# Kernel optimization log

Hardware: AMD Instinct MI355X
Metric: run time of the kernel (lower is better)

The kernel has to match this reference:

```python
import jax, jax.numpy as jnp
import numpy as np

B, C, F, T = 4, 64, 257, 256
H, OUT = 256, 64

def setup_inputs() -> dict:
    key = jax.random.key(0)
    ks = jax.random.split(key, 7)
    w = lambda k, shape: jax.random.normal(k, shape, dtype=jnp.float32) * 0.05
    return {
        "x": jax.random.normal(ks[0], (B, C, F, T), dtype=jnp.float32),
        "W_ih": w(ks[1], (4 * H, C)),   # torch LSTM weight_ih_l0, gate order i,f,g,o
        "W_hh": w(ks[2], (4 * H, H)),   # weight_hh_l0
        "b_ih": w(ks[3], (4 * H,)),
        "b_hh": w(ks[4], (4 * H,)),
        "W_lin": w(ks[5], (OUT, H)),
        "b_lin": w(ks[6], (OUT,)),
    }

def _lstm(y, W_ih, W_hh, b_ih, b_hh):
    # y: (N, T, C) -> (N, T, H); PyTorch gate order i, f, g, o
    N, Tl, _ = y.shape
    Hd = W_hh.shape[1]
    # precompute input contributions for all timesteps in one big GEMM
    x_gates = jnp.einsum('ntc,gc->ntg', y, W_ih) + b_ih + b_hh  # (N, T, 4H)

    def step(carry, xg):
        h, c = carry
        g = xg + h @ W_hh.T  # (N, 4H)
        i, f, gg, o = jnp.split(g, 4, axis=-1)
        c = jax.nn.sigmoid(f) * c + jax.nn.sigmoid(i) * jnp.tanh(gg)
        h = jax.nn.sigmoid(o) * jnp.tanh(c)
        return (h, c), h

    h0 = jnp.zeros((N, Hd), y.dtype)
    _, hs = jax.lax.scan(step, (h0, h0), jnp.swapaxes(x_gates, 0, 1))  # (T, N, H)
    return jnp.swapaxes(hs, 0, 1)  # (N, T, H)

def reference(x, W_ih, W_hh, b_ih, b_hh, W_lin, b_lin):
    b, c, f, t = x.shape
    y = x.transpose(0, 2, 3, 1).reshape(b * f, t, c)  # (B*F, T, C)
    h = _lstm(y, W_ih, W_hh, b_ih, b_hh)              # (B*F, T, H)
    out = h @ W_lin.T + b_lin                          # (B*F, T, OUT)
    return out.reshape(b, f, t, -1).transpose(0, 3, 1, 2)  # (B, OUT, F, T)
```

## Files before the change

kernel.cpp:

```cpp
#include <hip/hip_runtime.h>

#define NSEQ 1028
#define TT   256
#define CC   64
#define HH   256
#define SLABE 32768
#define XROW 528
#define XG_A (16*XROW)
#define XG_LDS (2*XG_A + 2*SLABE*2)
#define AROWB 656
#define FB_LDS (2*16*AROWB + 2*SLABE*2)
#define OUTP_LDS (128*264*2 + 64*264*2)

typedef unsigned short u16;
typedef float  f32x4 __attribute__((ext_vector_type(4)));
typedef __bf16 v8bf  __attribute__((ext_vector_type(8)));

__device__ __forceinline__ u16 f2bf(float f){
  unsigned u = __builtin_bit_cast(unsigned, f);
  u += 0x7FFFu + ((u >> 16) & 1u);
  return (u16)(u >> 16);
}
__device__ __forceinline__ float sigm(float x){
  float t = __builtin_amdgcn_exp2f(-1.4426950408889634f * x);
  return __builtin_amdgcn_rcpf(1.0f + t);
}
__device__ __forceinline__ float tanh_f(float x){
  float a = __builtin_fabsf(x);
  float t = __builtin_amdgcn_exp2f(-2.885390081777927f * a);
  float r = (1.0f - t) * __builtin_amdgcn_rcpf(1.0f + t);
  return __builtin_copysignf(r, x);
}
__device__ __forceinline__ void mfma_a(f32x4& d, v8bf a, v8bf b){
  asm("v_mfma_f32_16x16x32_bf16 %0, %1, %2, %0" : "+v"(d) : "v"(a), "a"(b));
}
__device__ __forceinline__ void mfma_v(f32x4& d, v8bf a, v8bf b){
  asm("v_mfma_f32_16x16x32_bf16 %0, %1, %2, %0" : "+v"(d) : "v"(a), "v"(b));
}
__device__ __forceinline__ void soft_barrier(){
  asm volatile("s_waitcnt lgkmcnt(0)" ::: "memory");
  __builtin_amdgcn_sched_barrier(0);
  __builtin_amdgcn_s_barrier();
  __builtin_amdgcn_sched_barrier(0);
}

__global__ void k_pack_w(const float* __restrict__ Whh, const float* __restrict__ Wih,
                         u16* __restrict__ wpack){
  int idx = blockIdx.x*256 + threadIdx.x;
  if (idx >= 10*SLABE) return;
  int j    = idx & 7;
  int lane = (idx >> 3) & 63;
  int ct   = (idx >> 9) & 7;
  int w    = (idx >> 12) & 7;
  int kt   = idx >> 15;
  int col  = (ct >> 1)*256 + w*32 + (ct & 1)*16 + (lane & 15);
  int k    = kt*32 + (lane >> 4)*8 + j;
  float v  = (k < 256) ? Whh[col*256 + k] : Wih[col*64 + (k - 256)];
  wpack[idx] = f2bf(v);
}

__global__ void k_bias(const float* __restrict__ bi, const float* __restrict__ bh,
                       float* __restrict__ bias){
  int i = blockIdx.x*256 + threadIdx.x;
  if (i < 1024) bias[i] = bi[i] + bh[i];
}

__global__ void k_wlin(const float* __restrict__ Wl, u16* __restrict__ wlin){
  int i = blockIdx.x*256 + threadIdx.x;
  if (i >= 64*264) return;
  int col = i / 264, k = i % 264;
  wlin[i] = (k < 256) ? f2bf(Wl[col*256 + k]) : (u16)0;
}

__global__ void k_ytrans(const float* __restrict__ x, u16* __restrict__ ybuf){
  __shared__ u16 tile[64][257];
  int n = blockIdx.x, b = n / 257, f = n % 257, tid = threadIdx.x;
  for (int i = tid; i < 64*256; i += 256){
    int c = i >> 8, t = i & 255;
    tile[c][t] = f2bf(x[((size_t)(b*64 + c)*257 + f)*256 + t]);
  }
  __syncthreads();
  for (int i = tid; i < 256*64; i += 256){
    int t = i >> 6, c = i & 63;
    ybuf[((size_t)n*256 + t)*64 + c] = tile[c][t];
  }
}

__global__ __launch_bounds__(512) void k_xgates(const u16* __restrict__ wpack,
      const float* __restrict__ bias, const u16* __restrict__ ybuf,
      u16* __restrict__ xgs, int t0, int CH){
  __shared__ u16 yt[16*16*72];
  const int g = blockIdx.x, tb = blockIdx.y*16, n0 = g*16;
  const int tid = threadIdx.x, lane = tid & 63, w = tid >> 6;
  const int l15 = lane & 15, q = lane >> 4;

  v8bf wf[2][8];
  #pragma unroll
  for (int kf = 0; kf < 2; ++kf)
    #pragma unroll
    for (int ct = 0; ct < 8; ++ct)
      wf[kf][ct] = *(const v8bf*)(wpack + (((8 + kf)*8 + w)*8 + ct)*512 + lane*8);
  float biasr[8];
  #pragma unroll
  for (int ct = 0; ct < 8; ++ct)
    biasr[ct] = bias[(ct >> 1)*256 + w*32 + (ct & 1)*16 + l15];

  #pragma unroll
  for (int s = 0; s < 4; ++s){
    int i = tid + s*512;
    int seq = i >> 7, tt = (i >> 3) & 15, c8 = i & 7;
    uint4 v = {0u,0u,0u,0u};
    if (n0 + seq < NSEQ)
      v = *(const uint4*)(ybuf + ((size_t)(n0 + seq)*TT + t0 + tb + tt)*64 + c8*8);
    *(uint4*)(yt + tt*1152 + seq*72 + c8*8) = v;
  }
  __syncthreads();

  for (int tt = 0; tt < 16; ++tt){
    f32x4 acc[8];
    #pragma unroll
    for (int ct = 0; ct < 8; ++ct)
      acc[ct] = (f32x4){biasr[ct], biasr[ct], biasr[ct], biasr[ct]};
    v8bf a0 = *(const v8bf*)(yt + tt*1152 + l15*72 + q*8);
    v8bf a1 = *(const v8bf*)(yt + tt*1152 + l15*72 + 32 + q*8);
    #pragma unroll
    for (int ct = 0; ct < 8; ++ct){
      acc[ct] = __builtin_amdgcn_mfma_f32_16x16x32_bf16(a0, wf[0][ct], acc[ct], 0, 0, 0);
      acc[ct] = __builtin_amdgcn_mfma_f32_16x16x32_bf16(a1, wf[1][ct], acc[ct], 0, 0, 0);
    }
    unsigned dw[16];
    #pragma unroll
    for (int ct = 0; ct < 8; ++ct)
      #pragma unroll
      for (int p = 0; p < 2; ++p)
        dw[ct*2 + p] = (unsigned)f2bf(acc[ct][2*p]) | ((unsigned)f2bf(acc[ct][2*p + 1]) << 16);
    u16* dst = xgs + ((((size_t)g*CH + tb + tt)*8 + w)*64 + lane)*32;
    *(uint4*)(dst +  0) = (uint4){dw[0], dw[1], dw[2], dw[3]};
    *(uint4*)(dst +  8) = (uint4){dw[4], dw[5], dw[6], dw[7]};
    *(uint4*)(dst + 16) = (uint4){dw[8], dw[9], dw[10], dw[11]};
    *(uint4*)(dst + 24) = (uint4){dw[12], dw[13], dw[14], dw[15]};
  }
}

__global__ __launch_bounds__(512, 2) void k_lstm_xg(const u16* __restrict__ wpack,
      const u16* __restrict__ xgs, u16* __restrict__ hbuf, float* __restrict__ cbuf,
      int t0, int CH){
  extern __shared__ char smem[];
  char* lA = smem;
  u16*  lW = (u16*)(smem + 2*XG_A);
  const int tid = threadIdx.x, lane = tid & 63, w = tid >> 6;
  const int g = blockIdx.x, n0 = g*16;
  const int l15 = lane & 15, q = lane >> 4;
  const int srow = tid >> 5, schunk = tid & 31;

  v8bf wreg[4][8];
  #pragma unroll
  for (int kt = 0; kt < 4; ++kt)
    #pragma unroll
    for (int ct = 0; ct < 8; ++ct)
      wreg[kt][ct] = *(const v8bf*)(wpack + ((kt*8 + w)*8 + ct)*512 + lane*8);
  {
    const uint4* src = (const uint4*)(wpack + 4*SLABE);
    uint4* dst = (uint4*)lW;
    for (int i = tid; i < (2*SLABE)/8; i += 512) dst[i] = src[i];
  }
  {
    uint4 hv = {0u,0u,0u,0u};
    if (t0 > 0 && n0 + srow < NSEQ)
      hv = *(const uint4*)(hbuf + ((size_t)(n0 + srow)*TT + (t0 - 1))*HH + schunk*8);
    *(uint4*)(lA + (t0 & 1)*XG_A + srow*XROW + schunk*16) = hv;
  }
  f32x4 creg[2];
  creg[0] = (f32x4){0.f,0.f,0.f,0.f};
  creg[1] = (f32x4){0.f,0.f,0.f,0.f};
  if (t0 > 0){
    #pragma unroll
    for (int u = 0; u < 2; ++u)
      #pragma unroll
      for (int j = 0; j < 4; ++j){
        int row = 4*q + j, unit = w*32 + u*16 + l15;
        if (n0 + row < NSEQ) creg[u][j] = cbuf[(size_t)(n0 + row)*HH + unit];
      }
  }
  __syncthreads();

  const u16* wp = wpack;

  v8bf sbuf[8];
  uint4 xgv[4];
  {
    const u16* wpw0 = wp + w*4096 + lane*8;
    #pragma unroll
    for (int ct = 0; ct < 8; ++ct) sbuf[ct] = *(const v8bf*)(wpw0 + 6*SLABE + ct*512);
    const u16* xb = xgs + ((((size_t)g*CH + 0)*8 + w)*64 + lane)*32;
    xgv[0] = *(const uint4*)(xb +  0);
    xgv[1] = *(const uint4*)(xb +  8);
    xgv[2] = *(const uint4*)(xb + 16);
    xgv[3] = *(const uint4*)(xb + 24);
  }

  for (int t = t0; t < t0 + CH; ++t){
    char* Acur = lA + (t & 1)*XG_A;
    char* Anxt = lA + ((t + 1) & 1)*XG_A;
    asm("" : "+s"(wp));
    const u16* wpw = wp + w*4096 + lane*8;

    if (t > t0 && n0 + srow < NSEQ){
      uint4 hv = *(const uint4*)(Acur + srow*XROW + schunk*16);
      *(uint4*)(hbuf + ((size_t)(n0 + srow)*TT + (t - 1))*HH + schunk*8) = hv;
    }

    f32x4 acc[8];
    #pragma unroll
    for (int ct = 0; ct < 8; ++ct){
      #pragma unroll
      for (int p = 0; p < 2; ++p){
        unsigned u = ((const unsigned*)&xgv[(ct*2 + p) >> 2])[(ct*2 + p) & 3];
        acc[ct][2*p]     = __builtin_bit_cast(float, u << 16);
        acc[ct][2*p + 1] = __builtin_bit_cast(float, u & 0xffff0000u);
      }
    }
    asm volatile("s_nop 1"
      : "+v"(acc[0]), "+v"(acc[1]), "+v"(acc[2]), "+v"(acc[3]),
        "+v"(acc[4]), "+v"(acc[5]), "+v"(acc[6]), "+v"(acc[7]));

    if (t + 1 < t0 + CH){
      const u16* xb = xgs + ((((size_t)g*CH + (t + 1 - t0))*8 + w)*64 + lane)*32;
      xgv[0] = *(const uint4*)(xb +  0);
      xgv[1] = *(const uint4*)(xb +  8);
      xgv[2] = *(const uint4*)(xb + 16);
      xgv[3] = *(const uint4*)(xb + 24);
    }
    __builtin_amdgcn_sched_barrier(0);

    #define AFRAGX(kt) (*(const v8bf*)(Acur + l15*XROW + (kt)*64 + q*16))
    #define LFRAGX(kt,ct) (*(const v8bf*)(lW + (((kt)-4)*8 + w)*4096 + (ct)*512 + lane*8))

    { v8bf a = AFRAGX(6);
      #pragma unroll
      for (int ct = 0; ct < 8; ++ct) mfma_v(acc[ct], a, sbuf[ct]);
      #pragma unroll
      for (int ct = 0; ct < 8; ++ct) sbuf[ct] = *(const v8bf*)(wpw + 7*SLABE + ct*512);
      __builtin_amdgcn_sched_barrier(0); }
    { v8bf a = AFRAGX(0);
      #pragma unroll
      for (int ct = 0; ct < 8; ++ct) mfma_a(acc[ct], a, wreg[0][ct]); }
    { v8bf a = AFRAGX(1);
      #pragma unroll
      for (int ct = 0; ct < 8; ++ct) mfma_a(acc[ct], a, wreg[1][ct]); }
    { v8bf a = AFRAGX(2);
      #pragma unroll
      for (int ct = 0; ct < 8; ++ct) mfma_a(acc[ct], a, wreg[2][ct]); }
    { v8bf a = AFRAGX(3);
      #pragma unroll
      for (int ct = 0; ct < 8; ++ct) mfma_a(acc[ct], a, wreg[3][ct]); }
    { v8bf a = AFRAGX(4);
      #pragma unroll
      for (int ct = 0; ct < 8; ++ct) mfma_v(acc[ct], a, LFRAGX(4,ct)); }
    { v8bf a = AFRAGX(5);
      #pragma unroll
      for (int ct = 0; ct < 8; ++ct) mfma_v(acc[ct], a, LFRAGX(5,ct)); }
    { v8bf a = AFRAGX(7);
      #pragma unroll
      for (int ct = 0; ct < 8; ++ct) mfma_v(acc[ct], a, sbuf[ct]);
      #pragma unroll
      for (int ct = 0; ct < 8; ++ct) sbuf[ct] = *(const v8bf*)(wpw + 6*SLABE + ct*512);
      __builtin_amdgcn_sched_barrier(0); }

    asm volatile("s_nop 7\n\ts_nop 7\n\ts_nop 7"
      : "+v"(acc[0]), "+v"(acc[1]), "+v"(acc[2]), "+v"(acc[3]),
        "+v"(acc[4]), "+v"(acc[5]), "+v"(acc[6]), "+v"(acc[7]));

    #pragma unroll
    for (int u = 0; u < 2; ++u){
      #pragma unroll
      for (int j = 0; j < 4; ++j){
        float xi = acc[0 + u][j], xf = acc[2 + u][j], xg = acc[4 + u][j], xo = acc[6 + u][j];
        float cv = sigm(xf)*creg[u][j] + sigm(xi)*tanh_f(xg);
        float hv = sigm(xo)*tanh_f(cv);
        creg[u][j] = cv;
        int row = 4*q + j, unit = w*32 + u*16 + l15;
        *(u16*)(Anxt + row*XROW + unit*2) = f2bf(hv);
      }
    }
    soft_barrier();
  }
  {
    char* Afin = lA + ((t0 + CH) & 1)*XG_A;
    if (n0 + srow < NSEQ){
      uint4 hv = *(const uint4*)(Afin + srow*XROW + schunk*16);
      *(uint4*)(hbuf + ((size_t)(n0 + srow)*TT + (t0 + CH - 1))*HH + schunk*8) = hv;
    }
    #pragma unroll
    for (int u = 0; u < 2; ++u)
      #pragma unroll
      for (int j = 0; j < 4; ++j){
        int row = 4*q + j, unit = w*32 + u*16 + l15;
        if (n0 + row < NSEQ) cbuf[(size_t)(n0 + row)*HH + unit] = creg[u][j];
      }
  }
}

__global__ __launch_bounds__(512, 2) void k_lstm_fb(const u16* __restrict__ wpack,
      const float* __restrict__ bias, const u16* __restrict__ ybuf,
      u16* __restrict__ hbuf){
  extern __shared__ char smem[];
  char* lA = smem;
  u16*  lW = (u16*)(smem + 2*16*AROWB);
  const int tid = threadIdx.x, lane = tid & 63, w = tid >> 6;
  const int n0 = blockIdx.x * 16;
  const int l15 = lane & 15, q = lane >> 4;
  const int srow = tid >> 5, schunk = tid & 31;

  v8bf wreg[4][8];
  #pragma unroll
  for (int kt = 0; kt < 4; ++kt)
    #pragma unroll
    for (int ct = 0; ct < 8; ++ct)
      wreg[kt][ct] = *(const v8bf*)(wpack + ((kt*8 + w)*8 + ct)*512 + lane*8);
  {
    const uint4* src = (const uint4*)(wpack + 4*SLABE);
    uint4* dst = (uint4*)lW;
    for (int i = tid; i < (2*SLABE)/8; i += 512) dst[i] = src[i];
  }
  float biasr[8];
  #pragma unroll
  for (int ct = 0; ct < 8; ++ct)
    biasr[ct] = bias[(ct >> 1)*256 + w*32 + (ct & 1)*16 + l15];
  {
    unsigned* z = (unsigned*)lA;
    for (int i = tid; i < (2*16*AROWB)/4; i += 512) z[i] = 0;
  }
  __syncthreads();
  {
    unsigned v = 0;
    if (n0 + srow < NSEQ)
      v = *(const unsigned*)(ybuf + ((size_t)(n0 + srow)*TT + 0)*64 + schunk*2);
    *(unsigned*)(lA + srow*AROWB + 512 + schunk*4) = v;
  }
  f32x4 creg[2];
  creg[0] = (f32x4){0.f,0.f,0.f,0.f};
  creg[1] = (f32x4){0.f,0.f,0.f,0.f};
  __syncthreads();

  const u16* wp = wpack;
  v8bf sbuf[8];
  {
    const u16* wpw0 = wp + w*4096 + lane*8;
    #pragma unroll
    for (int ct = 0; ct < 8; ++ct) sbuf[ct] = *(const v8bf*)(wpw0 + 6*SLABE + ct*512);
  }

  for (int t = 0; t < TT; ++t){
    char* Acur = lA + (t & 1)*16*AROWB;
    char* Anxt = lA + ((t + 1) & 1)*16*AROWB;
    asm("" : "+s"(wp));
    const u16* wpw = wp + w*4096 + lane*8;

    unsigned yv = 0;
    if (t + 1 < TT && n0 + srow < NSEQ)
      yv = *(const unsigned*)(ybuf + ((size_t)(n0 + srow)*TT + (t + 1))*64 + schunk*2);

    if (t >= 1 && n0 + srow < NSEQ){
      uint4 hv = *(const uint4*)(Acur + srow*AROWB + schunk*16);
      *(uint4*)(hbuf + ((size_t)(n0 + srow)*TT + (t - 1))*HH + schunk*8) = hv;
    }

    f32x4 acc[8];
    #pragma unroll
    for (int ct = 0; ct < 8; ++ct)
      acc[ct] = (f32x4){biasr[ct], biasr[ct], biasr[ct], biasr[ct]};
    asm volatile("s_nop 1"
      : "+v"(acc[0]), "+v"(acc[1]), "+v"(acc[2]), "+v"(acc[3]),
        "+v"(acc[4]), "+v"(acc[5]), "+v"(acc[6]), "+v"(acc[7]));

    #define AFRAG(kt) (*(const v8bf*)(Acur + l15*AROWB + (kt)*64 + q*16))
    #define LFRAG(kt,ct) (*(const v8bf*)(lW + (((kt)-4)*8 + w)*4096 + (ct)*512 + lane*8))

    { v8bf a = AFRAG(0);
      #pragma unroll
      for (int ct = 0; ct < 8; ++ct) mfma_a(acc[ct], a, wreg[0][ct]); }
    { v8bf a = AFRAG(1);
      #pragma unroll
      for (int ct = 0; ct < 8; ++ct) mfma_a(acc[ct], a, wreg[1][ct]); }
    { v8bf a = AFRAG(6);
      #pragma unroll
      for (int ct = 0; ct < 8; ++ct) mfma_v(acc[ct], a, sbuf[ct]);
      #pragma unroll
      for (int ct = 0; ct < 8; ++ct) sbuf[ct] = *(const v8bf*)(wpw + 7*SLABE + ct*512);
      __builtin_amdgcn_sched_barrier(0); }
    { v8bf a = AFRAG(2);
      #pragma unroll
      for (int ct = 0; ct < 8; ++ct) mfma_a(acc[ct], a, wreg[2][ct]); }
    { v8bf a = AFRAG(3);
      #pragma unroll
      for (int ct = 0; ct < 8; ++ct) mfma_a(acc[ct], a, wreg[3][ct]); }
    { v8bf a = AFRAG(7);
      #pragma unroll
      for (int ct = 0; ct < 8; ++ct) mfma_v(acc[ct], a, sbuf[ct]);
      #pragma unroll
      for (int ct = 0; ct < 8; ++ct) sbuf[ct] = *(const v8bf*)(wpw + 8*SLABE + ct*512);
      __builtin_amdgcn_sched_barrier(0); }
    { v8bf a = AFRAG(4);
      #pragma unroll
      for (int ct = 0; ct < 8; ++ct) mfma_v(acc[ct], a, LFRAG(4,ct)); }
    { v8bf a = AFRAG(8);
      #pragma unroll
      for (int ct = 0; ct < 8; ++ct) mfma_v(acc[ct], a, sbuf[ct]);
      #pragma unroll
      for (int ct = 0; ct < 8; ++ct) sbuf[ct] = *(const v8bf*)(wpw + 9*SLABE + ct*512);
      __builtin_amdgcn_sched_barrier(0); }
    { v8bf a = AFRAG(5);
      #pragma unroll
      for (int ct = 0; ct < 8; ++ct) mfma_v(acc[ct], a, LFRAG(5,ct)); }
    { v8bf a = AFRAG(9);
      #pragma unroll
      for (int ct = 0; ct < 8; ++ct) mfma_v(acc[ct], a, sbuf[ct]);
      #pragma unroll
      for (int ct = 0; ct < 8; ++ct) sbuf[ct] = *(const v8bf*)(wpw + 6*SLABE + ct*512);
      __builtin_amdgcn_sched_barrier(0); }

    asm volatile("s_nop 7\n\ts_nop 7\n\ts_nop 7"
      : "+v"(acc[0]), "+v"(acc[1]), "+v"(acc[2]), "+v"(acc[3]),
        "+v"(acc[4]), "+v"(acc[5]), "+v"(acc[6]), "+v"(acc[7]));

    #pragma unroll
    for (int u = 0; u < 2; ++u){
      #pragma unroll
      for (int j = 0; j < 4; ++j){
        float xi = acc[0 + u][j], xf = acc[2 + u][j], xg = acc[4 + u][j], xo = acc[6 + u][j];
        float cv = sigm(xf)*creg[u][j] + sigm(xi)*tanh_f(xg);
        float hv = sigm(xo)*tanh_f(cv);
        creg[u][j] = cv;
        int row = 4*q + j, unit = w*32 + u*16 + l15;
        *(u16*)(Anxt + row*AROWB + unit*2) = f2bf(hv);
      }
    }
    if (t + 1 < TT)
      *(unsigned*)(Anxt + srow*AROWB + 512 + schunk*4) = yv;
    soft_barrier();
  }
  {
    char* Afin = lA + (TT & 1)*16*AROWB;
    if (n0 + srow < NSEQ){
      uint4 hv = *(const uint4*)(Afin + srow*AROWB + schunk*16);
      *(uint4*)(hbuf + ((size_t)(n0 + srow)*TT + (TT - 1))*HH + schunk*8) = hv;
    }
  }
}

__global__ __launch_bounds__(256) void k_outproj(const u16* __restrict__ hbuf,
      const u16* __restrict__ wlin, const float* __restrict__ blin,
      float* __restrict__ out){
  extern __shared__ char smem[];
  u16* sA = (u16*)smem;
  u16* sB = (u16*)(smem + 128*264*2);
  const int n = blockIdx.x, th = blockIdx.y, t0 = th*128;
  const int b = n / 257, f = n % 257;
  const int tid = threadIdx.x, lane = tid & 63, wv = tid >> 6;

  for (int i = tid; i < 128*32; i += 256){
    int r = i >> 5, part = i & 31;
    *(uint4*)(sA + r*264 + part*8) =
        *(const uint4*)(hbuf + ((size_t)n*TT + t0 + r)*HH + part*8);
  }
  for (int i = tid; i < (64*264)/2; i += 256)
    ((unsigned*)sB)[i] = ((const unsigned*)wlin)[i];
  __syncthreads();

  f32x4 acc[2][4];
  #pragma unroll
  for (int m = 0; m < 2; ++m)
    #pragma unroll
    for (int nt = 0; nt < 4; ++nt){
      float bv = blin[nt*16 + (lane & 15)];
      acc[m][nt] = (f32x4){bv, bv, bv, bv};
    }
  const int khi = (lane >> 4) * 8;
  #pragma unroll
  for (int kt = 0; kt < 8; ++kt){
    v8bf av[2];
    #pragma unroll
    for (int m = 0; m < 2; ++m){
      int mt = wv*2 + m;
      av[m] = *(const v8bf*)(sA + (mt*16 + (lane & 15))*264 + kt*32 + khi);
    }
    #pragma unroll
    for (int nt = 0; nt < 4; ++nt){
      v8bf bv = *(const v8bf*)(sB + (nt*16 + (lane & 15))*264 + kt*32 + khi);
      #pragma unroll
      for (int m = 0; m < 2; ++m)
        acc[m][nt] = __builtin_amdgcn_mfma_f32_16x16x32_bf16(av[m], bv, acc[m][nt], 0, 0, 0);
    }
  }
  #pragma unroll
  for (int m = 0; m < 2; ++m){
    int mt = wv*2 + m;
    #pragma unroll
    for (int nt = 0; nt < 4; ++nt){
      int o = nt*16 + (lane & 15);
      int tb = t0 + mt*16 + 4*(lane >> 4);
      *(f32x4*)(out + (((size_t)b*64 + o)*257 + f)*TT + tb) = acc[m][nt];
    }
  }
}

extern "C" void kernel_launch(void* const* d_in, const int* in_sizes, int n_in,
                              void* d_out, int out_size, void* d_ws, size_t ws_size,
                              hipStream_t stream) {
  const float* x   = (const float*)d_in[0];
  const float* Wih = (const float*)d_in[1];
  const float* Whh = (const float*)d_in[2];
  const float* bih = (const float*)d_in[3];
  const float* bhh = (const float*)d_in[4];
  const float* Wl  = (const float*)d_in[5];
  const float* bl  = (const float*)d_in[6];
  float* out = (float*)d_out;

  char* p = (char*)d_ws;
  u16*   wpack = (u16*)p;   p += 655360;
  float* bias  = (float*)p; p += 4096;
  u16*   wlin  = (u16*)p;   p += 33792;
  float* cbuf  = (float*)p; p += (size_t)NSEQ*HH*4;
  u16*   ybuf  = (u16*)p;   p += (size_t)NSEQ*TT*CC*2;
  u16*   hbuf  = (u16*)p;   p += (size_t)NSEQ*TT*HH*2;
  u16*   xgs   = (u16*)p;
  const size_t BASE = (size_t)(p - (char*)d_ws);

  int CH = 0;
  if      (ws_size >= BASE + 65ull*64*32768) CH = 64;
  else if (ws_size >= BASE + 65ull*32*32768) CH = 32;
  else if (ws_size >= BASE + 65ull*16*32768) CH = 16;

  hipFuncSetAttribute((const void*)k_lstm_xg, hipFuncAttributeMaxDynamicSharedMemorySize, XG_LDS);
  hipFuncSetAttribute((const void*)k_lstm_fb, hipFuncAttributeMaxDynamicSharedMemorySize, FB_LDS);
  hipFuncSetAttribute((const void*)k_outproj, hipFuncAttributeMaxDynamicSharedMemorySize, OUTP_LDS);

  k_pack_w <<<1280, 256, 0, stream>>>(Whh, Wih, wpack);
  k_bias   <<<4,    256, 0, stream>>>(bih, bhh, bias);
  k_wlin   <<<66,   256, 0, stream>>>(Wl, wlin);
  k_ytrans <<<1028, 256, 0, stream>>>(x, ybuf);

  if (CH) {
    for (int t0 = 0; t0 < TT; t0 += CH){
      k_xgates <<<dim3(65, CH/16), 512, 0, stream>>>(wpack, bias, ybuf, xgs, t0, CH);
      k_lstm_xg<<<65, 512, XG_LDS, stream>>>(wpack, xgs, hbuf, cbuf, t0, CH);
    }
  } else {
    k_lstm_fb<<<65, 512, FB_LDS, stream>>>(wpack, bias, ybuf, hbuf);
  }
  k_outproj<<<dim3(1028, 2), 256, OUTP_LDS, stream>>>(hbuf, wlin, bl, out);
}
```

Before: 1.263 ms.

## Fuse input-gate GEMM into persistent LSTM kernel with per-block chunked xgates buffer

Replaces the alternating per-chunk k_xgates and k_lstm_xg launches with a single persistent kernel. Each 16-sequence block computes its own input-gate projections for a 32-step chunk into a private global buffer, then runs the recurrence over that chunk, and repeats. This removes the repeated kernel launches, the reload of weights into registers and LDS per chunk, and the cbuf save/restore of the cell state. In exchange, the input GEMM is now serialized inside the recurrent blocks with only 65 blocks active, so it no longer gets its own wider grid, and a drain barrier is added between phases.

```diff
diff --git a/kernel.cpp b/kernel.cpp
--- a/kernel.cpp
+++ b/kernel.cpp
@@ -4,10 +4,12 @@
 #define TT   256
 #define CC   64
 #define HH   256
+#define CH   32
 #define SLABE 32768
 #define XROW 528
 #define XG_A (16*XROW)
-#define XG_LDS (2*XG_A + 2*SLABE*2)
+#define LYS  1040
+#define XG_LDS (2*XG_A + 8192 + 2*SLABE*2)
 #define AROWB 656
 #define FB_LDS (2*16*AROWB + 2*SLABE*2)
 #define OUTP_LDS (128*264*2 + 64*264*2)
@@ -39,6 +41,12 @@
 }
 __device__ __forceinline__ void soft_barrier(){
   asm volatile("s_waitcnt lgkmcnt(0)" ::: "memory");
+  __builtin_amdgcn_sched_barrier(0);
+  __builtin_amdgcn_s_barrier();
+  __builtin_amdgcn_sched_barrier(0);
+}
+__device__ __forceinline__ void drain_barrier(){
+  asm volatile("s_waitcnt vmcnt(0) lgkmcnt(0)" ::: "memory");
   __builtin_amdgcn_sched_barrier(0);
   __builtin_amdgcn_s_barrier();
   __builtin_amdgcn_sched_barrier(0);
@@ -86,72 +94,18 @@
   }
 }
 
-__global__ __launch_bounds__(512) void k_xgates(const u16* __restrict__ wpack,
+__global__ __launch_bounds__(512, 2) void k_lstm_f(const u16* __restrict__ wpack,
       const float* __restrict__ bias, const u16* __restrict__ ybuf,
-      u16* __restrict__ xgs, int t0, int CH){
-  __shared__ u16 yt[16*16*72];
-  const int g = blockIdx.x, tb = blockIdx.y*16, n0 = g*16;
-  const int tid = threadIdx.x, lane = tid & 63, w = tid >> 6;
-  const int l15 = lane & 15, q = lane >> 4;
-
-  v8bf wf[2][8];
-  #pragma unroll
-  for (int kf = 0; kf < 2; ++kf)
-    #pragma unroll
-    for (int ct = 0; ct < 8; ++ct)
-      wf[kf][ct] = *(const v8bf*)(wpack + (((8 + kf)*8 + w)*8 + ct)*512 + lane*8);
-  float biasr[8];
-  #pragma unroll
-  for (int ct = 0; ct < 8; ++ct)
-    biasr[ct] = bias[(ct >> 1)*256 + w*32 + (ct & 1)*16 + l15];
-
-  #pragma unroll
-  for (int s = 0; s < 4; ++s){
-    int i = tid + s*512;
-    int seq = i >> 7, tt = (i >> 3) & 15, c8 = i & 7;
-    uint4 v = {0u,0u,0u,0u};
-    if (n0 + seq < NSEQ)
-      v = *(const uint4*)(ybuf + ((size_t)(n0 + seq)*TT + t0 + tb + tt)*64 + c8*8);
-    *(uint4*)(yt + tt*1152 + seq*72 + c8*8) = v;
-  }
-  __syncthreads();
-
-  for (int tt = 0; tt < 16; ++tt){
-    f32x4 acc[8];
-    #pragma unroll
-    for (int ct = 0; ct < 8; ++ct)
-      acc[ct] = (f32x4){biasr[ct], biasr[ct], biasr[ct], biasr[ct]};
-    v8bf a0 = *(const v8bf*)(yt + tt*1152 + l15*72 + q*8);
-    v8bf a1 = *(const v8bf*)(yt + tt*1152 + l15*72 + 32 + q*8);
-    #pragma unroll
-    for (int ct = 0; ct < 8; ++ct){
-      acc[ct] = __builtin_amdgcn_mfma_f32_16x16x32_bf16(a0, wf[0][ct], acc[ct], 0, 0, 0);
-      acc[ct] = __builtin_amdgcn_mfma_f32_16x16x32_bf16(a1, wf[1][ct], acc[ct], 0, 0, 0);
-    }
-    unsigned dw[16];
-    #pragma unroll
-    for (int ct = 0; ct < 8; ++ct)
-      #pragma unroll
-      for (int p = 0; p < 2; ++p)
-        dw[ct*2 + p] = (unsigned)f2bf(acc[ct][2*p]) | ((unsigned)f2bf(acc[ct][2*p + 1]) << 16);
-    u16* dst = xgs + ((((size_t)g*CH + tb + tt)*8 + w)*64 + lane)*32;
-    *(uint4*)(dst +  0) = (uint4){dw[0], dw[1], dw[2], dw[3]};
-    *(uint4*)(dst +  8) = (uint4){dw[4], dw[5], dw[6], dw[7]};
-    *(uint4*)(dst + 16) = (uint4){dw[8], dw[9], dw[10], dw[11]};
-    *(uint4*)(dst + 24) = (uint4){dw[12], dw[13], dw[14], dw[15]};
-  }
-}
-
-__global__ __launch_bounds__(512, 2) void k_lstm_xg(const u16* __restrict__ wpack,
-      const u16* __restrict__ xgs, u16* __restrict__ hbuf, float* __restrict__ cbuf,
-      int t0, int CH){
+      u16* __restrict__ xgb, u16* __restrict__ hbuf){
   extern __shared__ char smem[];
   char* lA = smem;
-  u16*  lW = (u16*)(smem + 2*XG_A);
+  char* lY = smem + XG_A;
+  u16*  lW = (u16*)(smem + 2*XG_A + 8192);
   const int tid = threadIdx.x, lane = tid & 63, w = tid >> 6;
   const int g = blockIdx.x, n0 = g*16;
   const int l15 = lane & 15, q = lane >> 4;
   const int srow = tid >> 5, schunk = tid & 31;
+  const int yc8 = tid & 7, yt3 = (tid >> 3) & 7, yseq0 = tid >> 6, yseq1 = (tid >> 6) + 8;
 
   v8bf wreg[4][8];
   #pragma unroll
@@ -164,140 +118,192 @@
     uint4* dst = (uint4*)lW;
     for (int i = tid; i < (2*SLABE)/8; i += 512) dst[i] = src[i];
   }
-  {
-    uint4 hv = {0u,0u,0u,0u};
-    if (t0 > 0 && n0 + srow < NSEQ)
-      hv = *(const uint4*)(hbuf + ((size_t)(n0 + srow)*TT + (t0 - 1))*HH + schunk*8);
-    *(uint4*)(lA + (t0 & 1)*XG_A + srow*XROW + schunk*16) = hv;
+  float biasr[8];
+  #pragma unroll
+  for (int ct = 0; ct < 8; ++ct)
+    biasr[ct] = bias[(ct >> 1)*256 + w*32 + (ct & 1)*16 + l15];
+  {
+    unsigned* z = (unsigned*)lA;
+    for (int i = tid; i < XG_A/4; i += 512) z[i] = 0;
   }
   f32x4 creg[2];
   creg[0] = (f32x4){0.f,0.f,0.f,0.f};
   creg[1] = (f32x4){0.f,0.f,0.f,0.f};
-  if (t0 > 0){
-    #pragma unroll
-    for (int u = 0; u < 2; ++u)
-      #pragma unroll
-      for (int j = 0; j < 4; ++j){
-        int row = 4*q + j, unit = w*32 + u*16 + l15;
-        if (n0 + row < NSEQ) creg[u][j] = cbuf[(size_t)(n0 + row)*HH + unit];
-      }
-  }
   __syncthreads();
 
   const u16* wp = wpack;
-
-  v8bf sbuf[8];
-  uint4 xgv[4];
-  {
-    const u16* wpw0 = wp + w*4096 + lane*8;
-    #pragma unroll
-    for (int ct = 0; ct < 8; ++ct) sbuf[ct] = *(const v8bf*)(wpw0 + 6*SLABE + ct*512);
-    const u16* xb = xgs + ((((size_t)g*CH + 0)*8 + w)*64 + lane)*32;
-    xgv[0] = *(const uint4*)(xb +  0);
-    xgv[1] = *(const uint4*)(xb +  8);
-    xgv[2] = *(const uint4*)(xb + 16);
-    xgv[3] = *(const uint4*)(xb + 24);
-  }
-
-  for (int t = t0; t < t0 + CH; ++t){
-    char* Acur = lA + (t & 1)*XG_A;
-    char* Anxt = lA + ((t + 1) & 1)*XG_A;
+  u16* xgblk = xgb + (size_t)g * (CH*16384);
+
+  for (int t0 = 0; t0 < TT; t0 += CH){
+    {
+      v8bf wf0[8], wf1[8];
+      #pragma unroll
+      for (int ct = 0; ct < 8; ++ct){
+        wf0[ct] = *(const v8bf*)(wpack + ((8*8 + w)*8 + ct)*512 + lane*8);
+        wf1[ct] = *(const v8bf*)(wpack + ((9*8 + w)*8 + ct)*512 + lane*8);
+      }
+      for (int tb = 0; tb < CH; tb += 8){
+        uint4 v0 = {0,0,0,0}, v1 = {0,0,0,0};
+        if (n0 + yseq0 < NSEQ)
+          v0 = *(const uint4*)(ybuf + ((size_t)(n0+yseq0)*TT + t0+tb+yt3)*64 + yc8*8);
+        if (n0 + yseq1 < NSEQ)
+          v1 = *(const uint4*)(ybuf + ((size_t)(n0+yseq1)*TT + t0+tb+yt3)*64 + yc8*8);
+        soft_barrier();
+        *(uint4*)(lY + yseq0*LYS + yt3*128 + yc8*16) = v0;
+        *(uint4*)(lY + yseq1*LYS + yt3*128 + yc8*16) = v1;
+        soft_barrier();
+        #pragma unroll
+        for (int tt = 0; tt < 8; ++tt){
+          v8bf a0 = *(const v8bf*)(lY + l15*LYS + tt*128 + q*16);
+          v8bf a1 = *(const v8bf*)(lY + l15*LYS + tt*128 + 64 + q*16);
+          u16* dst = xgblk + ((((size_t)(tb+tt))*8 + w)*64 + lane)*32;
+          {
+            f32x4 xa[4];
+            #pragma unroll
+            for (int c = 0; c < 4; ++c){
+              xa[c] = (f32x4){biasr[c], biasr[c], biasr[c], biasr[c]};
+              xa[c] = __builtin_amdgcn_mfma_f32_16x16x32_bf16(a0, wf0[c], xa[c], 0,0,0);
+              xa[c] = __builtin_amdgcn_mfma_f32_16x16x32_bf16(a1, wf1[c], xa[c], 0,0,0);
+            }
+            unsigned d[8];
+            #pragma unroll
+            for (int c = 0; c < 4; ++c){
+              d[c*2]   = (unsigned)f2bf(xa[c][0]) | ((unsigned)f2bf(xa[c][1]) << 16);
+              d[c*2+1] = (unsigned)f2bf(xa[c][2]) | ((unsigned)f2bf(xa[c][3]) << 16);
+            }
+            *(uint4*)(dst)     = (uint4){d[0], d[1], d[2], d[3]};
+            *(uint4*)(dst + 8) = (uint4){d[4], d[5], d[6], d[7]};
+          }
+          {
+            f32x4 xa[4];
+            #pragma unroll
+            for (int c = 0; c < 4; ++c){
+              xa[c] = (f32x4){biasr[c+4], biasr[c+4], biasr[c+4], biasr[c+4]};
+              xa[c] = __builtin_amdgcn_mfma_f32_16x16x32_bf16(a0, wf0[c+4], xa[c], 0,0,0);
+              xa[c] = __builtin_amdgcn_mfma_f32_16x16x32_bf16(a1, wf1[c+4], xa[c], 0,0,0);
+            }
+            unsigned d[8];
+            #pragma unroll
+            for (int c = 0; c < 4; ++c){
+              d[c*2]   = (unsigned)f2bf(xa[c][0]) | ((unsigned)f2bf(xa[c][1]) << 16);
+              d[c*2+1] = (unsigned)f2bf(xa[c][2]) | ((unsigned)f2bf(xa[c][3]) << 16);
+            }
+            *(uint4*)(dst + 16) = (uint4){d[0], d[1], d[2], d[3]};
+            *(uint4*)(dst + 24) = (uint4){d[4], d[5], d[6], d[7]};
+          }
+        }
+      }
+    }
+    drain_barrier();
+
     asm("" : "+s"(wp));
-    const u16* wpw = wp + w*4096 + lane*8;
-
-    if (t > t0 && n0 + srow < NSEQ){
-      uint4 hv = *(const uint4*)(Acur + srow*XROW + schunk*16);
-      *(uint4*)(hbuf + ((size_t)(n0 + srow)*TT + (t - 1))*HH + schunk*8) = hv;
-    }
-
-    f32x4 acc[8];
-    #pragma unroll
-    for (int ct = 0; ct < 8; ++ct){
-      #pragma unroll
-      for (int p = 0; p < 2; ++p){
-        unsigned u = ((const unsigned*)&xgv[(ct*2 + p) >> 2])[(ct*2 + p) & 3];
-        acc[ct][2*p]     = __builtin_bit_cast(float, u << 16);
-        acc[ct][2*p + 1] = __builtin_bit_cast(float, u & 0xffff0000u);
-      }
-    }
-    asm volatile("s_nop 1"
-      : "+v"(acc[0]), "+v"(acc[1]), "+v"(acc[2]), "+v"(acc[3]),
-        "+v"(acc[4]), "+v"(acc[5]), "+v"(acc[6]), "+v"(acc[7]));
-
-    if (t + 1 < t0 + CH){
-      const u16* xb = xgs + ((((size_t)g*CH + (t + 1 - t0))*8 + w)*64 + lane)*32;
+    v8bf sbuf[8];
+    uint4 xgv[4];
+    {
+      const u16* wpw0 = wp + w*4096 + lane*8;
+      #pragma unroll
+      for (int ct = 0; ct < 8; ++ct) sbuf[ct] = *(const v8bf*)(wpw0 + 6*SLABE + ct*512);
+      const u16* xb = xgblk + ((0*8 + w)*64 + lane)*32;
       xgv[0] = *(const uint4*)(xb +  0);
       xgv[1] = *(const uint4*)(xb +  8);
       xgv[2] = *(const uint4*)(xb + 16);
       xgv[3] = *(const uint4*)(xb + 24);
     }
-    __builtin_amdgcn_sched_barrier(0);
-
-    #define AFRAGX(kt) (*(const v8bf*)(Acur + l15*XROW + (kt)*64 + q*16))
-    #define LFRAGX(kt,ct) (*(const v8bf*)(lW + (((kt)-4)*8 + w)*4096 + (ct)*512 + lane*8))
-
-    { v8bf a = AFRAGX(6);
-      #pragma unroll
-      for (int ct = 0; ct < 8; ++ct) mfma_v(acc[ct], a, sbuf[ct]);
-      #pragma unroll
-      for (int ct = 0; ct < 8; ++ct) sbuf[ct] = *(const v8bf*)(wpw + 7*SLABE + ct*512);
-      __builtin_amdgcn_sched_barrier(0); }
-    { v8bf a = AFRAGX(0);
-      #pragma unroll
-      for (int ct = 0; ct < 8; ++ct) mfma_a(acc[ct], a, wreg[0][ct]); }
-    { v8bf a = AFRAGX(1);
-      #pragma unroll
-      for (int ct = 0; ct < 8; ++ct) mfma_a(acc[ct], a, wreg[1][ct]); }
-    { v8bf a = AFRAGX(2);
-      #pragma unroll
-      for (int ct = 0; ct < 8; ++ct) mfma_a(acc[ct], a, wreg[2][ct]); }
-    { v8bf a = AFRAGX(3);
-      #pragma unroll
-      for (int ct = 0; ct < 8; ++ct) mfma_a(acc[ct], a, wreg[3][ct]); }
-    { v8bf a = AFRAGX(4);
-      #pragma unroll
-      for (int ct = 0; ct < 8; ++ct) mfma_v(acc[ct], a, LFRAGX(4,ct)); }
-    { v8bf a = AFRAGX(5);
-      #pragma unroll
-      for (int ct = 0; ct < 8; ++ct) mfma_v(acc[ct], a, LFRAGX(5,ct)); }
-    { v8bf a = AFRAGX(7);
-      #pragma unroll
-      for (int ct = 0; ct < 8; ++ct) mfma_v(acc[ct], a, sbuf[ct]);
-      #pragma unroll
-      for (int ct = 0; ct < 8; ++ct) sbuf[ct] = *(const v8bf*)(wpw + 6*SLABE + ct*512);
-      __builtin_amdgcn_sched_barrier(0); }
-
-    asm volatile("s_nop 7\n\ts_nop 7\n\ts_nop 7"
-      : "+v"(acc[0]), "+v"(acc[1]), "+v"(acc[2]), "+v"(acc[3]),
-        "+v"(acc[4]), "+v"(acc[5]), "+v"(acc[6]), "+v"(acc[7]));
-
-    #pragma unroll
-    for (int u = 0; u < 2; ++u){
-      #pragma unroll
-      for (int j = 0; j < 4; ++j){
-        float xi = acc[0 + u][j], xf = acc[2 + u][j], xg = acc[4 + u][j], xo = acc[6 + u][j];
-        float cv = sigm(xf)*creg[u][j] + sigm(xi)*tanh_f(xg);
-        float hv = sigm(xo)*tanh_f(cv);
-        creg[u][j] = cv;
-        int row = 4*q + j, unit = w*32 + u*16 + l15;
-        *(u16*)(Anxt + row*XROW + unit*2) = f2bf(hv);
-      }
-    }
-    soft_barrier();
-  }
-  {
-    char* Afin = lA + ((t0 + CH) & 1)*XG_A;
+
+    for (int tl = 0; tl < CH; ++tl){
+      const int t = t0 + tl;
+      char* Acur = lA + (t & 1)*XG_A;
+      char* Anxt = lA + ((t + 1) & 1)*XG_A;
+      asm("" : "+s"(wp));
+      const u16* wpw = wp + w*4096 + lane*8;
+
+      if (t >= 1 && n0 + srow < NSEQ){
+        uint4 hv = *(const uint4*)(Acur + srow*XROW + schunk*16);
+        *(uint4*)(hbuf + ((size_t)(n0 + srow)*TT + (t - 1))*HH + schunk*8) = hv;
+      }
+
+      f32x4 acc[8];
+      #pragma unroll
+      for (int ct = 0; ct < 8; ++ct){
+        #pragma unroll
+        for (int p = 0; p < 2; ++p){
+          unsigned u = ((const unsigned*)&xgv[(ct*2 + p) >> 2])[(ct*2 + p) & 3];
+          acc[ct][2*p]     = __builtin_bit_cast(float, u << 16);
+          acc[ct][2*p + 1] = __builtin_bit_cast(float, u & 0xffff0000u);
+        }
+      }
+      asm volatile("s_nop 1"
+        : "+v"(acc[0]), "+v"(acc[1]), "+v"(acc[2]), "+v"(acc[3]),
+          "+v"(acc[4]), "+v"(acc[5]), "+v"(acc[6]), "+v"(acc[7]));
+
+      if (tl + 1 < CH){
+        const u16* xb = xgblk + ((((size_t)(tl + 1))*8 + w)*64 + lane)*32;
+        xgv[0] = *(const uint4*)(xb +  0);
+        xgv[1] = *(const uint4*)(xb +  8);
+        xgv[2] = *(const uint4*)(xb + 16);
+        xgv[3] = *(const uint4*)(xb + 24);
+      }
+      __builtin_amdgcn_sched_barrier(0);
+
+      #define AFX(kt) (*(const v8bf*)(Acur + l15*XROW + (kt)*64 + q*16))
+      #define LFX(kt,ct) (*(const v8bf*)(lW + (((kt)-4)*8 + w)*4096 + (ct)*512 + lane*8))
+
+      { v8bf a = AFX(6);
+        #pragma unroll
+        for (int ct = 0; ct < 8; ++ct) mfma_v(acc[ct], a, sbuf[ct]);
+        #pragma unroll
+        for (int ct = 0; ct < 8; ++ct) sbuf[ct] = *(const v8bf*)(wpw + 7*SLABE + ct*512);
+        __builtin_amdgcn_sched_barrier(0); }
+      { v8bf a = AFX(0);
+        #pragma unroll
+        for (int ct = 0; ct < 8; ++ct) mfma_a(acc[ct], a, wreg[0][ct]); }
+      { v8bf a = AFX(1);
+        #pragma unroll
+        for (int ct = 0; ct < 8; ++ct) mfma_a(acc[ct], a, wreg[1][ct]); }
+      { v8bf a = AFX(2);
+        #pragma unroll
+        for (int ct = 0; ct < 8; ++ct) mfma_a(acc[ct], a, wreg[2][ct]); }
+      { v8bf a = AFX(3);
+        #pragma unroll
+        for (int ct = 0; ct < 8; ++ct) mfma_a(acc[ct], a, wreg[3][ct]); }
+      { v8bf a = AFX(4);
+        #pragma unroll
+        for (int ct = 0; ct < 8; ++ct) mfma_v(acc[ct], a, LFX(4,ct)); }
+      { v8bf a = AFX(5);
+        #pragma unroll
+        for (int ct = 0; ct < 8; ++ct) mfma_v(acc[ct], a, LFX(5,ct)); }
+      { v8bf a = AFX(7);
+        #pragma unroll
+        for (int ct = 0; ct < 8; ++ct) mfma_v(acc[ct], a, sbuf[ct]);
+        #pragma unroll
+        for (int ct = 0; ct < 8; ++ct) sbuf[ct] = *(const v8bf*)(wpw + 6*SLABE + ct*512);
+        __builtin_amdgcn_sched_barrier(0); }
+
+      asm volatile("s_nop 7\n\ts_nop 7\n\ts_nop 7"
+        : "+v"(acc[0]), "+v"(acc[1]), "+v"(acc[2]), "+v"(acc[3]),
+          "+v"(acc[4]), "+v"(acc[5]), "+v"(acc[6]), "+v"(acc[7]));
+
+      #pragma unroll
+      for (int u = 0; u < 2; ++u){
+        #pragma unroll
+        for (int j = 0; j < 4; ++j){
+          float xi = acc[0 + u][j], xf = acc[2 + u][j], xg = acc[4 + u][j], xo = acc[6 + u][j];
+          float cv = sigm(xf)*creg[u][j] + sigm(xi)*tanh_f(xg);
+          float hv = sigm(xo)*tanh_f(cv);
+          creg[u][j] = cv;
+          int row = 4*q + j, unit = w*32 + u*16 + l15;
+          *(u16*)(Anxt + row*XROW + unit*2) = f2bf(hv);
+        }
+      }
+      soft_barrier();
+    }
+  }
+  {
+    char* Afin = lA + (TT & 1)*XG_A;
     if (n0 + srow < NSEQ){
       uint4 hv = *(const uint4*)(Afin + srow*XROW + schunk*16);
-      *(uint4*)(hbuf + ((size_t)(n0 + srow)*TT + (t0 + CH - 1))*HH + schunk*8) = hv;
-    }
-    #pragma unroll
-    for (int u = 0; u < 2; ++u)
-      #pragma unroll
-      for (int j = 0; j < 4; ++j){
-        int row = 4*q + j, unit = w*32 + u*16 + l15;
-        if (n0 + row < NSEQ) cbuf[(size_t)(n0 + row)*HH + unit] = creg[u][j];
-      }
+      *(uint4*)(hbuf + ((size_t)(n0 + srow)*TT + (TT - 1))*HH + schunk*8) = hv;
+    }
   }
 }
 
@@ -521,18 +527,12 @@
   u16*   wpack = (u16*)p;   p += 655360;
   float* bias  = (float*)p; p += 4096;
   u16*   wlin  = (u16*)p;   p += 33792;
-  float* cbuf  = (float*)p; p += (size_t)NSEQ*HH*4;
   u16*   ybuf  = (u16*)p;   p += (size_t)NSEQ*TT*CC*2;
   u16*   hbuf  = (u16*)p;   p += (size_t)NSEQ*TT*HH*2;
-  u16*   xgs   = (u16*)p;
-  const size_t BASE = (size_t)(p - (char*)d_ws);
-
-  int CH = 0;
-  if      (ws_size >= BASE + 65ull*64*32768) CH = 64;
-  else if (ws_size >= BASE + 65ull*32*32768) CH = 32;
-  else if (ws_size >= BASE + 65ull*16*32768) CH = 16;
-
-  hipFuncSetAttribute((const void*)k_lstm_xg, hipFuncAttributeMaxDynamicSharedMemorySize, XG_LDS);
+  u16*   xgb   = (u16*)p;
+  const size_t NEED = (size_t)(p - (char*)d_ws) + 65ull*CH*16384*2;
+
+  hipFuncSetAttribute((const void*)k_lstm_f,  hipFuncAttributeMaxDynamicSharedMemorySize, XG_LDS);
   hipFuncSetAttribute((const void*)k_lstm_fb, hipFuncAttributeMaxDynamicSharedMemorySize, FB_LDS);
   hipFuncSetAttribute((const void*)k_outproj, hipFuncAttributeMaxDynamicSharedMemorySize, OUTP_LDS);
 
@@ -541,13 +541,10 @@
   k_wlin   <<<66,   256, 0, stream>>>(Wl, wlin);
   k_ytrans <<<1028, 256, 0, stream>>>(x, ybuf);
 
-  if (CH) {
-    for (int t0 = 0; t0 < TT; t0 += CH){
-      k_xgates <<<dim3(65, CH/16), 512, 0, stream>>>(wpack, bias, ybuf, xgs, t0, CH);
-      k_lstm_xg<<<65, 512, XG_LDS, stream>>>(wpack, xgs, hbuf, cbuf, t0, CH);
-    }
-  } else {
+  if (ws_size >= NEED)
+    k_lstm_f <<<65, 512, XG_LDS, stream>>>(wpack, bias, ybuf, xgb, hbuf);
+  else
     k_lstm_fb<<<65, 512, FB_LDS, stream>>>(wpack, bias, ybuf, hbuf);
-  }
+
   k_outproj<<<dim3(1028, 2), 256, OUTP_LDS, stream>>>(hbuf, wlin, bl, out);
 }
```

After: 2.731 ms. 2.16x slower.
